# Kernel optimization log

Hardware: AMD Instinct MI355X
Metric: run time of the kernel (lower is better)

The kernel has to match this reference:

```python
import jax, jax.numpy as jnp
import numpy as np

ORDER = 2
BN_EPS = 1e-5

def setup_inputs() -> dict:
    key = jax.random.key(0)
    ks = jax.random.split(key, 8)
    B, N, L, H = 32, 512, 12, 64
    S = 2                      # support_len
    OUT = 64                   # out_dim
    M = ORDER * S * H          # einsum middle dim = 256
    x = jax.random.normal(ks[0], (B, N, L, H), dtype=jnp.float32)
    # row-scaled random diffusion matrices to keep multi-hop propagation stable
    support = jax.random.uniform(ks[1], (S, N, N), dtype=jnp.float32) / N
    scale = 1.0 / M
    weight = scale * jax.random.normal(ks[2], (L, M, OUT), dtype=jnp.float32)
    eps = jnp.zeros((1,), dtype=jnp.float32)
    gamma = jnp.ones((OUT,), dtype=jnp.float32)
    beta = jnp.zeros((OUT,), dtype=jnp.float32)
    w2 = jax.random.normal(ks[3], (OUT, OUT), dtype=jnp.float32) / np.sqrt(OUT)
    b2 = jnp.zeros((OUT,), dtype=jnp.float32)
    return {"x": x, "support": support, "weight": weight, "eps": eps,
            "gamma": gamma, "beta": beta, "w2": w2, "b2": b2}

def reference(x, support, weight, eps, gamma, beta, w2, b2):
    B, N, L, H = x.shape
    xv = x.reshape(B, N, L * H)            # [B,N,LH]
    res = []
    for i in range(support.shape[0]):      # small fixed loop over supports
        A = support[i]                     # [N,N]
        out = xv
        for _ in range(ORDER):
            out = (1.0 + eps) * out + jnp.einsum('nm,bmd->bnd', A, out)
            res.append(out)
    out = jnp.stack(res, axis=-1)          # [B,N,LH,K], K = order*support_len
    K = out.shape[-1]
    out = out.reshape(B, N, L, H * K)      # [B,N,L,M]
    out = jnp.einsum('bnlm,lmo->bno', out, weight)   # [B,N,OUT]
    # dropout is identity in eval mode
    C = out.shape[-1]
    flat = out.reshape(B * N, C)
    mean = flat.mean(axis=0)
    var = flat.var(axis=0)                 # biased, matching torch BN training
    normed = (flat - mean) * jax.lax.rsqrt(var + BN_EPS) * gamma + beta
    y = jax.nn.relu(normed.reshape(B, N, C))
    return jnp.einsum('bnc,oc->bno', y, w2) + b2
```

## Files before the change

kernel.cpp:

```cpp
#include <hip/hip_runtime.h>
#include <hip/hip_bf16.h>
#include <cstddef>
#include <cstdint>

#define B_   32
#define N_   512
#define D_   768
#define OUT_ 64
#define R_   (B_ * N_)

typedef unsigned short u16;
typedef __bf16 bf16x8 __attribute__((ext_vector_type(8)));
typedef float  f32x4  __attribute__((ext_vector_type(4)));
typedef unsigned short u16x8 __attribute__((ext_vector_type(8)));

__device__ __forceinline__ u16 f2bf(float f) {
    __hip_bfloat16 h = __float2bfloat16(f);
    return __builtin_bit_cast(u16, h);
}

__device__ __forceinline__ f32x4 mfma16(u16x8 a, u16x8 b, f32x4 c) {
    return __builtin_amdgcn_mfma_f32_16x16x32_bf16(
        __builtin_bit_cast(bf16x8, a), __builtin_bit_cast(bf16x8, b), c, 0, 0, 0);
}

__device__ __forceinline__ void gl2lds16(const void* g, void* l) {
    __builtin_amdgcn_global_load_lds(
        (const __attribute__((address_space(1))) unsigned int*)g,
        (__attribute__((address_space(3))) unsigned int*)l, 16, 0, 0);
}

__global__ __launch_bounds__(256) void prep2(
    const float* __restrict__ support, const float* __restrict__ weight,
    const float* __restrict__ epsp,
    u16* __restrict__ MallC, u16* __restrict__ MT, u16* __restrict__ Wt)
{
    const int blk = blockIdx.x, tid = threadIdx.x;
    __shared__ float t[32][33];
    if (blk < 512) {
        int s = blk >> 8, rem = blk & 255;
        int n0 = (rem >> 4) * 32, m0 = (rem & 15) * 32;
        const float f = 1.0f + epsp[0];
        const float* S = support + (size_t)s * 262144;
#pragma unroll
        for (int p = 0; p < 4; ++p) {
            int nl = p * 8 + (tid >> 5), ml = tid & 31;
            float v = S[(size_t)(n0 + nl) * 512 + m0 + ml];
            if (n0 + nl == m0 + ml) v += f;
            MallC[(size_t)(n0 + nl) * 2048 + s * 1024 + m0 + ml] = f2bf(v);
            t[nl][ml] = v;
        }
        __syncthreads();
#pragma unroll
        for (int p = 0; p < 4; ++p) {
            int ml = p * 8 + (tid >> 5), nl = tid & 31;
            MT[(size_t)s * 262144 + (size_t)(m0 + ml) * 512 + n0 + nl] = f2bf(t[nl][ml]);
        }
    } else {
        int idx = (blk - 512) * 256 + tid;
        int k = idx / 49152, rem = idx % 49152;
        int o = rem / 768, d = rem % 768;
        int l = d >> 6, hh = d & 63;
        Wt[idx] = f2bf(weight[((size_t)l * 256 + hh * 4 + k) * 64 + o]);
    }
}

__global__ __launch_bounds__(256) void zgemm_fused(
    const u16* __restrict__ Wt, const float* __restrict__ x,
    const u16* __restrict__ MallC_in, const u16* __restrict__ MT,
    u16* __restrict__ Z, u16* __restrict__ MallC_out)
{
    __shared__ __align__(16) char smem[32768];
    const int tid = threadIdx.x, lane = tid & 63, wid = tid >> 6;
    const int wr = wid >> 1, wc = wid & 1;
    const int lrow = lane & 15, lk = (lane >> 4) * 8;
    const int q = lane >> 4;
    const int bid = blockIdx.x;

    if (bid < 512) {
        u16* As = (u16*)smem;
        u16* Bs = (u16*)(smem + 16384);
        const int rt = bid >> 1, y = bid & 1;
        const int j0 = rt * 64;

        const u16* gsrcA[4]; u16* ldstA[4];
#pragma unroll
        for (int t = 0; t < 4; ++t) {
            int idx = wid * 4 + t;
            int pan = idx >> 3, sub = idx & 7;
            gsrcA[t] = Wt + (size_t)(y * 128 + sub * 16 + lrow) * 768 + pan * 32 + lk;
            ldstA[t] = As + pan * 4096 + sub * 512;
        }
        const int brow = tid & 63, kp = tid >> 6;
        const f32x4* gx = (const f32x4*)(x + (size_t)(j0 + brow) * 768 + kp * 16);
        u16* bdst = Bs + (kp >> 1) * 2048 + (brow >> 4) * 512 + (brow & 15) * 8;
        const int bo0 = (kp & 1) * 2 * 128, bo1 = bo0 + 128;

        f32x4 acc[4][2] = {};
        for (int kk = 0; kk < 12; ++kk) {
#pragma unroll
            for (int t = 0; t < 4; ++t) gl2lds16(gsrcA[t], ldstA[t]);
#pragma unroll
            for (int t = 0; t < 4; ++t) gsrcA[t] += 64;
            f32x4 a0 = gx[0], a1 = gx[1], a2 = gx[2], a3 = gx[3];
            gx += 16;
            u16x8 w0, w1;
#pragma unroll
            for (int j = 0; j < 4; ++j) {
                w0[j] = f2bf(a0[j]); w0[4 + j] = f2bf(a1[j]);
                w1[j] = f2bf(a2[j]); w1[4 + j] = f2bf(a3[j]);
            }
            *(u16x8*)(bdst + bo0) = w0;
            *(u16x8*)(bdst + bo1) = w1;
            __syncthreads();
#pragma unroll
            for (int pan = 0; pan < 2; ++pan) {
                u16x8 af[4], bq[2];
#pragma unroll
                for (int f = 0; f < 4; ++f)
                    af[f] = *(const u16x8*)(As + pan * 4096 + (wr * 4 + f) * 512 + lane * 8);
#pragma unroll
                for (int f = 0; f < 2; ++f)
                    bq[f] = *(const u16x8*)(Bs + pan * 2048 + (wc * 2 + f) * 512 + lane * 8);
#pragma unroll
                for (int fi = 0; fi < 4; ++fi)
#pragma unroll
                    for (int fj = 0; fj < 2; ++fj)
                        acc[fi][fj] = mfma16(af[fi], bq[fj], acc[fi][fj]);
            }
            __syncthreads();
        }
        u16* Rw = (u16*)smem + wid * 2560;
#pragma unroll
        for (int fi = 0; fi < 4; ++fi)
#pragma unroll
            for (int fj = 0; fj < 2; ++fj)
#pragma unroll
                for (int r = 0; r < 4; ++r)
                    Rw[(fi * 16 + q * 4 + r) * 40 + fj * 16 + lrow] = f2bf(acc[fi][fj][r]);
        __syncthreads();
        const int k = y * 2 + wr;
        const int b = rt >> 3;
        const int m0 = (j0 & 511) + wc * 32;
#pragma unroll
        for (int p = 0; p < 4; ++p) {
            int row = p * 16 + (lane >> 2);
            int cc = (lane & 3) * 8;
            u16x8 v = *(const u16x8*)(Rw + row * 40 + cc);
            *(u16x8*)(Z + (size_t)(b * 64 + row) * 2048 + k * 512 + m0 + cc) = v;
        }
    } else {
        u16* St = (u16*)smem;
        int lb = bid - 512;
        int s = lb >> 4, rem = lb & 15;
        int i0 = (rem >> 2) * 128, j0 = (rem & 3) * 128;
        const u16* Ab = MallC_in + s * 1024;
        const u16* Bb = MT + (size_t)s * 262144;

        const u16* gsrc[8]; u16* ldst[8];
#pragma unroll
        for (int t = 0; t < 8; ++t) {
            int idx = wid * 8 + t;
            int pan = idx >> 4, q2 = idx & 15;
            if (q2 < 8) {
                gsrc[t] = Ab + (size_t)(i0 + q2 * 16 + lrow) * 2048 + pan * 32 + lk;
                ldst[t] = St + pan * 8192 + q2 * 512;
            } else {
                gsrc[t] = Bb + (size_t)(j0 + (q2 - 8) * 16 + lrow) * 512 + pan * 32 + lk;
                ldst[t] = St + pan * 8192 + 4096 + (q2 - 8) * 512;
            }
        }
        f32x4 acc[4][4] = {};
        for (int kk = 0; kk < 8; ++kk) {
#pragma unroll
            for (int t = 0; t < 8; ++t) gl2lds16(gsrc[t], ldst[t]);
#pragma unroll
            for (int t = 0; t < 8; ++t) gsrc[t] += 64;
            __syncthreads();
#pragma unroll
            for (int pan = 0; pan < 2; ++pan) {
                u16x8 af[4], bq[4];
#pragma unroll
                for (int f = 0; f < 4; ++f)
                    af[f] = *(const u16x8*)(St + pan * 8192 + (wr * 4 + f) * 512 + lane * 8);
#pragma unroll
                for (int f = 0; f < 4; ++f)
                    bq[f] = *(const u16x8*)(St + pan * 8192 + 4096 + (wc * 4 + f) * 512 + lane * 8);
#pragma unroll
                for (int fi = 0; fi < 4; ++fi)
#pragma unroll
                    for (int fj = 0; fj < 4; ++fj)
                        acc[fi][fj] = mfma16(af[fi], bq[fj], acc[fi][fj]);
            }
            __syncthreads();
        }
#pragma unroll
        for (int fi = 0; fi < 4; ++fi)
#pragma unroll
            for (int fj = 0; fj < 4; ++fj)
#pragma unroll
                for (int r = 0; r < 4; ++r) {
                    int n = i0 + wr * 64 + fi * 16 + q * 4 + r;
                    int c = j0 + wc * 64 + fj * 16 + lrow;
                    MallC_out[(size_t)n * 2048 + (2 * s + 1) * 512 + c] = f2bf(acc[fi][fj][r]);
                }
    }
}

__global__ __launch_bounds__(256) void ysum(
    const u16* __restrict__ MallC, const u16* __restrict__ Z,
    float* __restrict__ Yh)
{
    __shared__ __align__(16) u16 St[8192];
    u16* As = St; u16* Bs = St + 4096;
    const int tid = threadIdx.x, lane = tid & 63, wid = tid >> 6;
    const int wr = wid >> 1, wc = wid & 1;
    const int lrow = lane & 15, lk = (lane >> 4) * 8;
    const int bid = blockIdx.x;
    const int rt = bid & 255, ks = bid >> 8;
    const int r0 = rt * 64, b = rt >> 3, n0 = r0 & 511;
    const size_t km0 = (size_t)ks * 1024;

    const u16* gsrc[4]; u16* ldst[4];
#pragma unroll
    for (int t = 0; t < 4; ++t) {
        int idx = wid * 4 + t;
        int pan = idx >> 3, q2 = idx & 7;
        if (q2 < 4) {
            gsrc[t] = MallC + (size_t)(n0 + q2 * 16 + lrow) * 2048 + km0 + pan * 32 + lk;
            ldst[t] = As + pan * 2048 + q2 * 512;
        } else {
            int s2 = q2 - 4;
            gsrc[t] = Z + (size_t)(b * 64 + s2 * 16 + lrow) * 2048 + km0 + pan * 32 + lk;
            ldst[t] = Bs + pan * 2048 + s2 * 512;
        }
    }
    f32x4 acc[2][2] = {};
    for (int kk = 0; kk < 16; ++kk) {
#pragma unroll
        for (int t = 0; t < 4; ++t) gl2lds16(gsrc[t], ldst[t]);
#pragma unroll
        for (int t = 0; t < 4; ++t) gsrc[t] += 64;
        __syncthreads();
#pragma unroll
        for (int pan = 0; pan < 2; ++pan) {
            u16x8 af[2], bq[2];
#pragma unroll
            for (int f = 0; f < 2; ++f)
                af[f] = *(const u16x8*)(As + pan * 2048 + (wr * 2 + f) * 512 + lane * 8);
#pragma unroll
            for (int f = 0; f < 2; ++f)
                bq[f] = *(const u16x8*)(Bs + pan * 2048 + (wc * 2 + f) * 512 + lane * 8);
#pragma unroll
            for (int fi = 0; fi < 2; ++fi)
#pragma unroll
                for (int fj = 0; fj < 2; ++fj)
                    acc[fi][fj] = mfma16(af[fi], bq[fj], acc[fi][fj]);
        }
        __syncthreads();
    }
    const int q = lane >> 4;
    float* Yk = Yh + (size_t)ks * R_ * 64;
#pragma unroll
    for (int fi = 0; fi < 2; ++fi)
#pragma unroll
        for (int fj = 0; fj < 2; ++fj)
#pragma unroll
            for (int r = 0; r < 4; ++r) {
                int rr = r0 + wr * 32 + fi * 16 + q * 4 + r;
                int o  = wc * 32 + fj * 16 + lrow;
                Yk[(size_t)rr * 64 + o] = acc[fi][fj][r];
            }
}

__global__ __launch_bounds__(256) void bn_part(
    const float* __restrict__ Yh, float* __restrict__ part)
{
    const int blk = blockIdx.x, tid = threadIdx.x;
    const int o = tid & 63, g = tid >> 6;
    float s = 0.f, s2 = 0.f;
#pragma unroll
    for (int p = 0; p < 16; ++p) {
        int r = blk * 64 + p * 4 + g;
        size_t off = (size_t)r * 64 + o;
        float v = Yh[off] + Yh[(size_t)R_ * 64 + off];
        s += v; s2 += v * v;
    }
    __shared__ float ls[4][64], ls2[4][64];
    ls[g][o] = s; ls2[g][o] = s2;
    __syncthreads();
    if (tid < 64) {
        float t = 0.f, t2 = 0.f;
#pragma unroll
        for (int g2 = 0; g2 < 4; ++g2) { t += ls[g2][tid]; t2 += ls2[g2][tid]; }
        part[blk * 128 + tid]      = t;
        part[blk * 128 + 64 + tid] = t2;
    }
}

__global__ __launch_bounds__(256) void bn_final(
    const float* __restrict__ part, const float* __restrict__ gamma,
    const float* __restrict__ beta, float* __restrict__ stats)
{
    const int tid = threadIdx.x;
    const int c = tid & 63, g = tid >> 6;
    float s = 0.f, s2 = 0.f;
    for (int b = g; b < 256; b += 4) {
        s  += part[b * 128 + c];
        s2 += part[b * 128 + 64 + c];
    }
    __shared__ float ls[4][64], ls2[4][64];
    ls[g][c] = s; ls2[g][c] = s2;
    __syncthreads();
    if (tid < 64) {
        float t = 0.f, t2 = 0.f;
#pragma unroll
        for (int g2 = 0; g2 < 4; ++g2) { t += ls[g2][tid]; t2 += ls2[g2][tid]; }
        float mean = t * (1.0f / R_);
        float var  = t2 * (1.0f / R_) - mean * mean;
        float a = rsqrtf(var + 1e-5f) * gamma[tid];
        stats[tid]      = a;
        stats[64 + tid] = beta[tid] - mean * a;
    }
}

__global__ __launch_bounds__(256) void bn_out(
    const float* __restrict__ Yh, const float* __restrict__ stats,
    const float* __restrict__ w2, const float* __restrict__ b2,
    float* __restrict__ out)
{
    __shared__ float ys[64 * 68];
    __shared__ float w2s[64 * 65];
    __shared__ float sa[64], sh[64];
    const int tid = threadIdx.x;
    const int r0 = blockIdx.x * 64;
#pragma unroll
    for (int i = 0; i < 16; ++i) {
        int idx = tid + i * 256;
        w2s[(idx >> 6) * 65 + (idx & 63)] = w2[idx];
    }
    if (tid < 64) { sa[tid] = stats[tid]; sh[tid] = stats[64 + tid]; }
    __syncthreads();
    const int o = tid & 63, g = tid >> 6;
    {
        float a = sa[o], b = sh[o];
#pragma unroll
        for (int p = 0; p < 16; ++p) {
            int rl = p * 4 + g;
            size_t off = (size_t)(r0 + rl) * 64 + o;
            float v = Yh[off] + Yh[(size_t)R_ * 64 + off];
            ys[o * 68 + rl] = fmaxf(fmaf(v, a, b), 0.f);
        }
    }
    __syncthreads();
    float acc[16];
    float bb = b2[o];
#pragma unroll
    for (int j = 0; j < 16; ++j) acc[j] = bb;
    for (int c = 0; c < 64; ++c) {
        float wv = w2s[o * 65 + c];
        const float* yr = ys + c * 68 + g * 16;
        f32x4 y0 = *(const f32x4*)(yr);
        f32x4 y1 = *(const f32x4*)(yr + 4);
        f32x4 y2 = *(const f32x4*)(yr + 8);
        f32x4 y3 = *(const f32x4*)(yr + 12);
#pragma unroll
        for (int j = 0; j < 4; ++j) {
            acc[j]      = fmaf(wv, y0[j], acc[j]);
            acc[4 + j]  = fmaf(wv, y1[j], acc[4 + j]);
            acc[8 + j]  = fmaf(wv, y2[j], acc[8 + j]);
            acc[12 + j] = fmaf(wv, y3[j], acc[12 + j]);
        }
    }
#pragma unroll
    for (int j = 0; j < 16; ++j)
        out[(size_t)(r0 + g * 16 + j) * OUT_ + o] = acc[j];
}

extern "C" void kernel_launch(void* const* d_in, const int* in_sizes, int n_in,
                              void* d_out, int out_size, void* d_ws, size_t ws_size,
                              hipStream_t stream)
{
    const float* x       = (const float*)d_in[0];
    const float* support = (const float*)d_in[1];
    const float* weight  = (const float*)d_in[2];
    const float* eps     = (const float*)d_in[3];
    const float* gamma   = (const float*)d_in[4];
    const float* beta    = (const float*)d_in[5];
    const float* w2      = (const float*)d_in[6];
    const float* b2      = (const float*)d_in[7];
    float* out = (float*)d_out;

    char* ws = (char*)d_ws;
    u16*   MallC = (u16*)(ws);
    u16*   MT    = (u16*)(ws + 2097152);
    u16*   Wt    = (u16*)(ws + 3145728);
    u16*   Z     = (u16*)(ws + 3538944);
    float* Yh    = (float*)(ws + 11927552);
    float* part  = (float*)(ws + 20316160);
    float* stats = (float*)(ws + 20447232);

    prep2     <<<1280, 256, 0, stream>>>(support, weight, eps, MallC, MT, Wt);
    zgemm_fused<<<544, 256, 0, stream>>>(Wt, x, MallC, MT, Z, MallC);
    ysum      <<<512,  256, 0, stream>>>(MallC, Z, Yh);
    bn_part   <<<256,  256, 0, stream>>>(Yh, part);
    bn_final  <<<1,    256, 0, stream>>>(part, gamma, beta, stats);
    bn_out    <<<256,  256, 0, stream>>>(Yh, stats, w2, b2, out);
}
```

Measured before the change: 172.7 us.

## Pre-convert x to bf16 and software-pipeline GEMM LDS loads with multi-buffering

Moves the fp32→bf16 conversion of x into the prep kernel, writing a bf16 copy to workspace so the Z GEMM can stream it with direct global-to-LDS loads. The Z GEMM gets double-buffered LDS with vmcnt waits and raw barriers. ysum gets triple-buffered prefetch two tiles ahead. Block indices are also remapped so related tiles share an XCD. This aims to hide global load latency behind MFMA work, at the cost of an extra full pass over x (read fp32, write bf16) and more shared memory per block.

```diff
diff --git a/kernel.cpp b/kernel.cpp
--- a/kernel.cpp
+++ b/kernel.cpp
@@ -14,6 +14,9 @@
 typedef float  f32x4  __attribute__((ext_vector_type(4)));
 typedef unsigned short u16x8 __attribute__((ext_vector_type(8)));
 
+#define WAITVM(n) __asm__ __volatile__("s_waitcnt vmcnt(" #n ")" ::: "memory")
+#define SBAR()    __builtin_amdgcn_s_barrier()
+
 __device__ __forceinline__ u16 f2bf(float f) {
     __hip_bfloat16 h = __float2bfloat16(f);
     return __builtin_bit_cast(u16, h);
@@ -30,15 +33,25 @@
         (__attribute__((address_space(3))) unsigned int*)l, 16, 0, 0);
 }
 
-__global__ __launch_bounds__(256) void prep2(
-    const float* __restrict__ support, const float* __restrict__ weight,
-    const float* __restrict__ epsp,
-    u16* __restrict__ MallC, u16* __restrict__ MT, u16* __restrict__ Wt)
+__global__ __launch_bounds__(256) void prep3(
+    const float* __restrict__ x, const float* __restrict__ support,
+    const float* __restrict__ weight, const float* __restrict__ epsp,
+    u16* __restrict__ xb, u16* __restrict__ MallC, u16* __restrict__ MT,
+    u16* __restrict__ Wt)
 {
     const int blk = blockIdx.x, tid = threadIdx.x;
     __shared__ float t[32][33];
-    if (blk < 512) {
-        int s = blk >> 8, rem = blk & 255;
+    if (blk < 6144) {
+        int i = (blk * 256 + tid) * 8;
+        f32x4 a = *(const f32x4*)(x + i);
+        f32x4 b = *(const f32x4*)(x + i + 4);
+        u16x8 o;
+#pragma unroll
+        for (int j = 0; j < 4; ++j) { o[j] = f2bf(a[j]); o[4 + j] = f2bf(b[j]); }
+        *(u16x8*)(xb + i) = o;
+    } else if (blk < 6656) {
+        int local = blk - 6144;
+        int s = local >> 8, rem = local & 255;
         int n0 = (rem >> 4) * 32, m0 = (rem & 15) * 32;
         const float f = 1.0f + epsp[0];
         const float* S = support + (size_t)s * 262144;
@@ -57,7 +70,7 @@
             MT[(size_t)s * 262144 + (size_t)(m0 + ml) * 512 + n0 + nl] = f2bf(t[nl][ml]);
         }
     } else {
-        int idx = (blk - 512) * 256 + tid;
+        int idx = (blk - 6656) * 256 + tid;
         int k = idx / 49152, rem = idx % 49152;
         int o = rem / 768, d = rem % 768;
         int l = d >> 6, hh = d & 63;
@@ -65,12 +78,13 @@
     }
 }
 
-__global__ __launch_bounds__(256) void zgemm_fused(
-    const u16* __restrict__ Wt, const float* __restrict__ x,
+__global__ __launch_bounds__(256) void zmsq(
+    const u16* __restrict__ Wt, const u16* __restrict__ xb,
     const u16* __restrict__ MallC_in, const u16* __restrict__ MT,
     u16* __restrict__ Z, u16* __restrict__ MallC_out)
 {
-    __shared__ __align__(16) char smem[32768];
+    __shared__ __align__(16) char smem[49152];
+    u16* SM = (u16*)smem;
     const int tid = threadIdx.x, lane = tid & 63, wid = tid >> 6;
     const int wr = wid >> 1, wc = wid & 1;
     const int lrow = lane & 15, lk = (lane >> 4) * 8;
@@ -78,57 +92,57 @@
     const int bid = blockIdx.x;
 
     if (bid < 512) {
-        u16* As = (u16*)smem;
-        u16* Bs = (u16*)(smem + 16384);
-        const int rt = bid >> 1, y = bid & 1;
-        const int j0 = rt * 64;
-
-        const u16* gsrcA[4]; u16* ldstA[4];
-#pragma unroll
-        for (int t = 0; t < 4; ++t) {
-            int idx = wid * 4 + t;
-            int pan = idx >> 3, sub = idx & 7;
-            gsrcA[t] = Wt + (size_t)(y * 128 + sub * 16 + lrow) * 768 + pan * 32 + lk;
-            ldstA[t] = As + pan * 4096 + sub * 512;
-        }
-        const int brow = tid & 63, kp = tid >> 6;
-        const f32x4* gx = (const f32x4*)(x + (size_t)(j0 + brow) * 768 + kp * 16);
-        u16* bdst = Bs + (kp >> 1) * 2048 + (brow >> 4) * 512 + (brow & 15) * 8;
-        const int bo0 = (kp & 1) * 2 * 128, bo1 = bo0 + 128;
+        const int j = bid & 7, y = (bid >> 3) & 1, g = bid >> 4;
+        const int rt = g * 8 + j;
+        const int b = rt >> 3;
+
+        const u16* gsrc[6]; int loff[6];
+#pragma unroll
+        for (int t = 0; t < 6; ++t) {
+            int idx = wid * 6 + t;
+            if (idx < 16) {
+                int pan = idx >> 3, sub = idx & 7;
+                gsrc[t] = Wt + (size_t)(y * 128 + sub * 16 + lrow) * 768 + pan * 32 + lk;
+                loff[t] = pan * 4096 + sub * 512;
+            } else {
+                int i2 = idx - 16;
+                int pan = i2 >> 2, sub = i2 & 3;
+                gsrc[t] = xb + (size_t)(rt * 64 + sub * 16 + lrow) * 768 + pan * 32 + lk;
+                loff[t] = 8192 + pan * 2048 + sub * 512;
+            }
+        }
+#pragma unroll
+        for (int t = 0; t < 6; ++t) { gl2lds16(gsrc[t], SM + loff[t]); gsrc[t] += 64; }
 
         f32x4 acc[4][2] = {};
+#pragma unroll
         for (int kk = 0; kk < 12; ++kk) {
-#pragma unroll
-            for (int t = 0; t < 4; ++t) gl2lds16(gsrcA[t], ldstA[t]);
-#pragma unroll
-            for (int t = 0; t < 4; ++t) gsrcA[t] += 64;
-            f32x4 a0 = gx[0], a1 = gx[1], a2 = gx[2], a3 = gx[3];
-            gx += 16;
-            u16x8 w0, w1;
-#pragma unroll
-            for (int j = 0; j < 4; ++j) {
-                w0[j] = f2bf(a0[j]); w0[4 + j] = f2bf(a1[j]);
-                w1[j] = f2bf(a2[j]); w1[4 + j] = f2bf(a3[j]);
-            }
-            *(u16x8*)(bdst + bo0) = w0;
-            *(u16x8*)(bdst + bo1) = w1;
-            __syncthreads();
+            if (kk < 11) {
+                u16* base = SM + ((kk + 1) & 1) * 12288;
+#pragma unroll
+                for (int t = 0; t < 6; ++t) { gl2lds16(gsrc[t], base + loff[t]); gsrc[t] += 64; }
+                WAITVM(6);
+            } else {
+                WAITVM(0);
+            }
+            SBAR();
+            const u16* base = SM + (kk & 1) * 12288;
 #pragma unroll
             for (int pan = 0; pan < 2; ++pan) {
                 u16x8 af[4], bq[2];
 #pragma unroll
                 for (int f = 0; f < 4; ++f)
-                    af[f] = *(const u16x8*)(As + pan * 4096 + (wr * 4 + f) * 512 + lane * 8);
+                    af[f] = *(const u16x8*)(base + pan * 4096 + (wr * 4 + f) * 512 + lane * 8);
 #pragma unroll
                 for (int f = 0; f < 2; ++f)
-                    bq[f] = *(const u16x8*)(Bs + pan * 2048 + (wc * 2 + f) * 512 + lane * 8);
+                    bq[f] = *(const u16x8*)(base + 8192 + pan * 2048 + (wc * 2 + f) * 512 + lane * 8);
 #pragma unroll
                 for (int fi = 0; fi < 4; ++fi)
 #pragma unroll
                     for (int fj = 0; fj < 2; ++fj)
                         acc[fi][fj] = mfma16(af[fi], bq[fj], acc[fi][fj]);
             }
-            __syncthreads();
+            SBAR();
         }
         u16* Rw = (u16*)smem + wid * 2560;
 #pragma unroll
@@ -140,8 +154,7 @@
                     Rw[(fi * 16 + q * 4 + r) * 40 + fj * 16 + lrow] = f2bf(acc[fi][fj][r]);
         __syncthreads();
         const int k = y * 2 + wr;
-        const int b = rt >> 3;
-        const int m0 = (j0 & 511) + wc * 32;
+        const int m0 = (rt & 7) * 64 + wc * 32;
 #pragma unroll
         for (int p = 0; p < 4; ++p) {
             int row = p * 16 + (lane >> 2);
@@ -150,7 +163,7 @@
             *(u16x8*)(Z + (size_t)(b * 64 + row) * 2048 + k * 512 + m0 + cc) = v;
         }
     } else {
-        u16* St = (u16*)smem;
+        u16* St = SM;
         int lb = bid - 512;
         int s = lb >> 4, rem = lb & 15;
         int i0 = (rem >> 2) * 128, j0 = (rem & 3) * 128;
@@ -211,53 +224,68 @@
     const u16* __restrict__ MallC, const u16* __restrict__ Z,
     float* __restrict__ Yh)
 {
-    __shared__ __align__(16) u16 St[8192];
-    u16* As = St; u16* Bs = St + 4096;
+    __shared__ __align__(16) u16 SM[24576];
     const int tid = threadIdx.x, lane = tid & 63, wid = tid >> 6;
     const int wr = wid >> 1, wc = wid & 1;
     const int lrow = lane & 15, lk = (lane >> 4) * 8;
     const int bid = blockIdx.x;
-    const int rt = bid & 255, ks = bid >> 8;
-    const int r0 = rt * 64, b = rt >> 3, n0 = r0 & 511;
+    const int xcd = bid & 7, tt = bid >> 3;
+    const int b = (tt >> 4) * 8 + xcd;
+    const int nt = (tt >> 1) & 7, ks = tt & 1;
+    const int n0 = nt * 64;
+    const int r0 = b * 512 + n0;
     const size_t km0 = (size_t)ks * 1024;
 
-    const u16* gsrc[4]; u16* ldst[4];
+    const u16* gsrc[4]; int loff[4];
 #pragma unroll
     for (int t = 0; t < 4; ++t) {
         int idx = wid * 4 + t;
-        int pan = idx >> 3, q2 = idx & 7;
-        if (q2 < 4) {
-            gsrc[t] = MallC + (size_t)(n0 + q2 * 16 + lrow) * 2048 + km0 + pan * 32 + lk;
-            ldst[t] = As + pan * 2048 + q2 * 512;
+        if (idx < 8) {
+            int pan = idx >> 2, sub = idx & 3;
+            gsrc[t] = MallC + (size_t)(n0 + sub * 16 + lrow) * 2048 + km0 + pan * 32 + lk;
+            loff[t] = pan * 2048 + sub * 512;
         } else {
-            int s2 = q2 - 4;
-            gsrc[t] = Z + (size_t)(b * 64 + s2 * 16 + lrow) * 2048 + km0 + pan * 32 + lk;
-            ldst[t] = Bs + pan * 2048 + s2 * 512;
-        }
+            int i2 = idx - 8;
+            int pan = i2 >> 2, sub = i2 & 3;
+            gsrc[t] = Z + (size_t)(b * 64 + sub * 16 + lrow) * 2048 + km0 + pan * 32 + lk;
+            loff[t] = 4096 + pan * 2048 + sub * 512;
+        }
+    }
+#pragma unroll
+    for (int st = 0; st < 2; ++st) {
+#pragma unroll
+        for (int t = 0; t < 4; ++t) { gl2lds16(gsrc[t], SM + st * 8192 + loff[t]); gsrc[t] += 64; }
     }
     f32x4 acc[2][2] = {};
+#pragma unroll
     for (int kk = 0; kk < 16; ++kk) {
-#pragma unroll
-        for (int t = 0; t < 4; ++t) gl2lds16(gsrc[t], ldst[t]);
-#pragma unroll
-        for (int t = 0; t < 4; ++t) gsrc[t] += 64;
-        __syncthreads();
+        int nxt = kk + 2;
+        if (nxt < 16) {
+            u16* base = SM + (nxt % 3) * 8192;
+#pragma unroll
+            for (int t = 0; t < 4; ++t) { gl2lds16(gsrc[t], base + loff[t]); gsrc[t] += 64; }
+        }
+        if (kk < 14) WAITVM(8);
+        else if (kk == 14) WAITVM(4);
+        else WAITVM(0);
+        SBAR();
+        const u16* base = SM + (kk % 3) * 8192;
 #pragma unroll
         for (int pan = 0; pan < 2; ++pan) {
             u16x8 af[2], bq[2];
 #pragma unroll
             for (int f = 0; f < 2; ++f)
-                af[f] = *(const u16x8*)(As + pan * 2048 + (wr * 2 + f) * 512 + lane * 8);
+                af[f] = *(const u16x8*)(base + pan * 2048 + (wr * 2 + f) * 512 + lane * 8);
 #pragma unroll
             for (int f = 0; f < 2; ++f)
-                bq[f] = *(const u16x8*)(Bs + pan * 2048 + (wc * 2 + f) * 512 + lane * 8);
+                bq[f] = *(const u16x8*)(base + 4096 + pan * 2048 + (wc * 2 + f) * 512 + lane * 8);
 #pragma unroll
             for (int fi = 0; fi < 2; ++fi)
 #pragma unroll
                 for (int fj = 0; fj < 2; ++fj)
                     acc[fi][fj] = mfma16(af[fi], bq[fj], acc[fi][fj]);
         }
-        __syncthreads();
+        SBAR();
     }
     const int q = lane >> 4;
     float* Yk = Yh + (size_t)ks * R_ * 64;
@@ -392,18 +420,19 @@
     float* out = (float*)d_out;
 
     char* ws = (char*)d_ws;
-    u16*   MallC = (u16*)(ws);
-    u16*   MT    = (u16*)(ws + 2097152);
-    u16*   Wt    = (u16*)(ws + 3145728);
-    u16*   Z     = (u16*)(ws + 3538944);
-    float* Yh    = (float*)(ws + 11927552);
-    float* part  = (float*)(ws + 20316160);
-    float* stats = (float*)(ws + 20447232);
-
-    prep2     <<<1280, 256, 0, stream>>>(support, weight, eps, MallC, MT, Wt);
-    zgemm_fused<<<544, 256, 0, stream>>>(Wt, x, MallC, MT, Z, MallC);
-    ysum      <<<512,  256, 0, stream>>>(MallC, Z, Yh);
-    bn_part   <<<256,  256, 0, stream>>>(Yh, part);
-    bn_final  <<<1,    256, 0, stream>>>(part, gamma, beta, stats);
-    bn_out    <<<256,  256, 0, stream>>>(Yh, stats, w2, b2, out);
-}
+    u16*   xb    = (u16*)(ws);
+    u16*   MallC = (u16*)(ws + 25165824);
+    u16*   MT    = (u16*)(ws + 27262976);
+    u16*   Wt    = (u16*)(ws + 28311552);
+    u16*   Z     = (u16*)(ws + 28704768);
+    float* Yh    = (float*)(ws + 37093376);
+    float* part  = (float*)(ws + 45481984);
+    float* stats = (float*)(ws + 45613056);
+
+    prep3   <<<7424, 256, 0, stream>>>(x, support, weight, eps, xb, MallC, MT, Wt);
+    zmsq    <<<544,  256, 0, stream>>>(Wt, xb, MallC, MT, Z, MallC);
+    ysum    <<<512,  256, 0, stream>>>(MallC, Z, Yh);
+    bn_part <<<256,  256, 0, stream>>>(Yh, part);
+    bn_final<<<1,    256, 0, stream>>>(part, gamma, beta, stats);
+    bn_out  <<<256,  256, 0, stream>>>(Yh, stats, w2, b2, out);
+}
```

Result: no change. 175.8 us (+1.8%).

## Load GEMM operands directly to registers with prefetch and 4-way split-K ysum

Applied to the files above, without the earlier changes.

The Z GEMM and the ysum GEMM no longer stage operands through LDS with block barriers. Each wave now loads its MFMA fragments straight from global memory into registers and prefetches the next k-step while the current one computes. ysum's tiling changes to 128-row by 64-column tiles with a 4-way K split instead of 2-way, so the BN kernels now sum four partial Yh buffers. This removes LDS traffic and syncs, but gives up cross-wave reuse of loaded tiles and writes and reads extra partial-sum memory.

```diff
diff --git a/kernel.cpp b/kernel.cpp
--- a/kernel.cpp
+++ b/kernel.cpp
@@ -65,70 +65,69 @@
     }
 }
 
-__global__ __launch_bounds__(256) void zgemm_fused(
+__global__ __launch_bounds__(256) void zmsq(
     const u16* __restrict__ Wt, const float* __restrict__ x,
     const u16* __restrict__ MallC_in, const u16* __restrict__ MT,
     u16* __restrict__ Z, u16* __restrict__ MallC_out)
 {
     __shared__ __align__(16) char smem[32768];
     const int tid = threadIdx.x, lane = tid & 63, wid = tid >> 6;
-    const int wr = wid >> 1, wc = wid & 1;
-    const int lrow = lane & 15, lk = (lane >> 4) * 8;
+    const int lrow = lane & 15, lk8 = (lane >> 4) * 8;
     const int q = lane >> 4;
     const int bid = blockIdx.x;
 
     if (bid < 512) {
-        u16* As = (u16*)smem;
-        u16* Bs = (u16*)(smem + 16384);
-        const int rt = bid >> 1, y = bid & 1;
-        const int j0 = rt * 64;
-
-        const u16* gsrcA[4]; u16* ldstA[4];
-#pragma unroll
-        for (int t = 0; t < 4; ++t) {
-            int idx = wid * 4 + t;
-            int pan = idx >> 3, sub = idx & 7;
-            gsrcA[t] = Wt + (size_t)(y * 128 + sub * 16 + lrow) * 768 + pan * 32 + lk;
-            ldstA[t] = As + pan * 4096 + sub * 512;
-        }
-        const int brow = tid & 63, kp = tid >> 6;
-        const f32x4* gx = (const f32x4*)(x + (size_t)(j0 + brow) * 768 + kp * 16);
-        u16* bdst = Bs + (kp >> 1) * 2048 + (brow >> 4) * 512 + (brow & 15) * 8;
-        const int bo0 = (kp & 1) * 2 * 128, bo1 = bo0 + 128;
+        const int y = bid & 1, mt = bid >> 1;
+        const int b = mt >> 3, m0 = (mt & 7) * 64;
+        const int wr = wid >> 1, wc = wid & 1;
+
+        const u16* ap[4];
+#pragma unroll
+        for (int fi = 0; fi < 4; ++fi)
+            ap[fi] = Wt + (size_t)(y * 128 + wr * 64 + fi * 16 + lrow) * 768 + lk8;
+        const float* bp[2];
+#pragma unroll
+        for (int fj = 0; fj < 2; ++fj)
+            bp[fj] = x + (size_t)(b * 512 + m0 + wc * 32 + fj * 16 + lrow) * 768 + lk8;
+
+        u16x8 Ar[4]; f32x4 Br0[2], Br1[2];
+#pragma unroll
+        for (int fi = 0; fi < 4; ++fi) Ar[fi] = *(const u16x8*)(ap[fi]);
+#pragma unroll
+        for (int fj = 0; fj < 2; ++fj) {
+            Br0[fj] = *(const f32x4*)(bp[fj]);
+            Br1[fj] = *(const f32x4*)(bp[fj] + 4);
+        }
 
         f32x4 acc[4][2] = {};
-        for (int kk = 0; kk < 12; ++kk) {
-#pragma unroll
-            for (int t = 0; t < 4; ++t) gl2lds16(gsrcA[t], ldstA[t]);
-#pragma unroll
-            for (int t = 0; t < 4; ++t) gsrcA[t] += 64;
-            f32x4 a0 = gx[0], a1 = gx[1], a2 = gx[2], a3 = gx[3];
-            gx += 16;
-            u16x8 w0, w1;
-#pragma unroll
-            for (int j = 0; j < 4; ++j) {
-                w0[j] = f2bf(a0[j]); w0[4 + j] = f2bf(a1[j]);
-                w1[j] = f2bf(a2[j]); w1[4 + j] = f2bf(a3[j]);
+#pragma unroll
+        for (int kk = 0; kk < 24; ++kk) {
+            u16x8 Bc[2];
+#pragma unroll
+            for (int fj = 0; fj < 2; ++fj) {
+                u16x8 w;
+#pragma unroll
+                for (int j = 0; j < 4; ++j) { w[j] = f2bf(Br0[fj][j]); w[4 + j] = f2bf(Br1[fj][j]); }
+                Bc[fj] = w;
             }
-            *(u16x8*)(bdst + bo0) = w0;
-            *(u16x8*)(bdst + bo1) = w1;
-            __syncthreads();
-#pragma unroll
-            for (int pan = 0; pan < 2; ++pan) {
-                u16x8 af[4], bq[2];
-#pragma unroll
-                for (int f = 0; f < 4; ++f)
-                    af[f] = *(const u16x8*)(As + pan * 4096 + (wr * 4 + f) * 512 + lane * 8);
-#pragma unroll
-                for (int f = 0; f < 2; ++f)
-                    bq[f] = *(const u16x8*)(Bs + pan * 2048 + (wc * 2 + f) * 512 + lane * 8);
-#pragma unroll
-                for (int fi = 0; fi < 4; ++fi)
-#pragma unroll
-                    for (int fj = 0; fj < 2; ++fj)
-                        acc[fi][fj] = mfma16(af[fi], bq[fj], acc[fi][fj]);
+            u16x8 Ac[4];
+#pragma unroll
+            for (int fi = 0; fi < 4; ++fi) Ac[fi] = Ar[fi];
+            if (kk < 23) {
+                const int d = (kk + 1) * 32;
+#pragma unroll
+                for (int fi = 0; fi < 4; ++fi) Ar[fi] = *(const u16x8*)(ap[fi] + d);
+#pragma unroll
+                for (int fj = 0; fj < 2; ++fj) {
+                    Br0[fj] = *(const f32x4*)(bp[fj] + d);
+                    Br1[fj] = *(const f32x4*)(bp[fj] + d + 4);
+                }
             }
-            __syncthreads();
+#pragma unroll
+            for (int fi = 0; fi < 4; ++fi)
+#pragma unroll
+                for (int fj = 0; fj < 2; ++fj)
+                    acc[fi][fj] = mfma16(Ac[fi], Bc[fj], acc[fi][fj]);
         }
         u16* Rw = (u16*)smem + wid * 2560;
 #pragma unroll
@@ -140,17 +139,16 @@
                     Rw[(fi * 16 + q * 4 + r) * 40 + fj * 16 + lrow] = f2bf(acc[fi][fj][r]);
         __syncthreads();
         const int k = y * 2 + wr;
-        const int b = rt >> 3;
-        const int m0 = (j0 & 511) + wc * 32;
 #pragma unroll
         for (int p = 0; p < 4; ++p) {
             int row = p * 16 + (lane >> 2);
             int cc = (lane & 3) * 8;
             u16x8 v = *(const u16x8*)(Rw + row * 40 + cc);
-            *(u16x8*)(Z + (size_t)(b * 64 + row) * 2048 + k * 512 + m0 + cc) = v;
+            *(u16x8*)(Z + (size_t)(b * 64 + row) * 2048 + k * 512 + m0 + wc * 32 + cc) = v;
         }
     } else {
         u16* St = (u16*)smem;
+        const int wr = wid >> 1, wc = wid & 1;
         int lb = bid - 512;
         int s = lb >> 4, rem = lb & 15;
         int i0 = (rem >> 2) * 128, j0 = (rem & 3) * 128;
@@ -163,10 +161,10 @@
             int idx = wid * 8 + t;
             int pan = idx >> 4, q2 = idx & 15;
             if (q2 < 8) {
-                gsrc[t] = Ab + (size_t)(i0 + q2 * 16 + lrow) * 2048 + pan * 32 + lk;
+                gsrc[t] = Ab + (size_t)(i0 + q2 * 16 + lrow) * 2048 + pan * 32 + lk8;
                 ldst[t] = St + pan * 8192 + q2 * 512;
             } else {
-                gsrc[t] = Bb + (size_t)(j0 + (q2 - 8) * 16 + lrow) * 512 + pan * 32 + lk;
+                gsrc[t] = Bb + (size_t)(j0 + (q2 - 8) * 16 + lrow) * 512 + pan * 32 + lk8;
                 ldst[t] = St + pan * 8192 + 4096 + (q2 - 8) * 512;
             }
         }
@@ -208,67 +206,61 @@
 }
 
 __global__ __launch_bounds__(256) void ysum(
-    const u16* __restrict__ MallC, const u16* __restrict__ Z,
-    float* __restrict__ Yh)
-{
-    __shared__ __align__(16) u16 St[8192];
-    u16* As = St; u16* Bs = St + 4096;
+    const u16* __restrict__ G, const u16* __restrict__ Z, float* __restrict__ Yh)
+{
     const int tid = threadIdx.x, lane = tid & 63, wid = tid >> 6;
-    const int wr = wid >> 1, wc = wid & 1;
-    const int lrow = lane & 15, lk = (lane >> 4) * 8;
+    const int lrow = lane & 15, lk8 = (lane >> 4) * 8;
+    const int q = lane >> 4;
     const int bid = blockIdx.x;
-    const int rt = bid & 255, ks = bid >> 8;
-    const int r0 = rt * 64, b = rt >> 3, n0 = r0 & 511;
-    const size_t km0 = (size_t)ks * 1024;
-
-    const u16* gsrc[4]; u16* ldst[4];
-#pragma unroll
-    for (int t = 0; t < 4; ++t) {
-        int idx = wid * 4 + t;
-        int pan = idx >> 3, q2 = idx & 7;
-        if (q2 < 4) {
-            gsrc[t] = MallC + (size_t)(n0 + q2 * 16 + lrow) * 2048 + km0 + pan * 32 + lk;
-            ldst[t] = As + pan * 2048 + q2 * 512;
-        } else {
-            int s2 = q2 - 4;
-            gsrc[t] = Z + (size_t)(b * 64 + s2 * 16 + lrow) * 2048 + km0 + pan * 32 + lk;
-            ldst[t] = Bs + pan * 2048 + s2 * 512;
-        }
-    }
-    f32x4 acc[2][2] = {};
+    const int kq = bid & 3, rt = bid >> 2;
+    const int b = rt >> 2, n0 = (rt & 3) * 128;
+    const int r0 = b * 512 + n0;
+
+    const u16* ap[2];
+#pragma unroll
+    for (int fi = 0; fi < 2; ++fi)
+        ap[fi] = G + (size_t)(n0 + wid * 32 + fi * 16 + lrow) * 2048 + kq * 512 + lk8;
+    const u16* bp[4];
+#pragma unroll
+    for (int fj = 0; fj < 4; ++fj)
+        bp[fj] = Z + (size_t)(b * 64 + fj * 16 + lrow) * 2048 + kq * 512 + lk8;
+
+    u16x8 Ar[2], Br[4];
+#pragma unroll
+    for (int fi = 0; fi < 2; ++fi) Ar[fi] = *(const u16x8*)(ap[fi]);
+#pragma unroll
+    for (int fj = 0; fj < 4; ++fj) Br[fj] = *(const u16x8*)(bp[fj]);
+
+    f32x4 acc[2][4] = {};
+#pragma unroll
     for (int kk = 0; kk < 16; ++kk) {
-#pragma unroll
-        for (int t = 0; t < 4; ++t) gl2lds16(gsrc[t], ldst[t]);
-#pragma unroll
-        for (int t = 0; t < 4; ++t) gsrc[t] += 64;
-        __syncthreads();
-#pragma unroll
-        for (int pan = 0; pan < 2; ++pan) {
-            u16x8 af[2], bq[2];
-#pragma unroll
-            for (int f = 0; f < 2; ++f)
-                af[f] = *(const u16x8*)(As + pan * 2048 + (wr * 2 + f) * 512 + lane * 8);
-#pragma unroll
-            for (int f = 0; f < 2; ++f)
-                bq[f] = *(const u16x8*)(Bs + pan * 2048 + (wc * 2 + f) * 512 + lane * 8);
-#pragma unroll
-            for (int fi = 0; fi < 2; ++fi)
-#pragma unroll
-                for (int fj = 0; fj < 2; ++fj)
-                    acc[fi][fj] = mfma16(af[fi], bq[fj], acc[fi][fj]);
-        }
-        __syncthreads();
-    }
-    const int q = lane >> 4;
-    float* Yk = Yh + (size_t)ks * R_ * 64;
+        u16x8 Ac[2], Bc[4];
+#pragma unroll
+        for (int fi = 0; fi < 2; ++fi) Ac[fi] = Ar[fi];
+#pragma unroll
+        for (int fj = 0; fj < 4; ++fj) Bc[fj] = Br[fj];
+        if (kk < 15) {
+            const int d = (kk + 1) * 32;
+#pragma unroll
+            for (int fi = 0; fi < 2; ++fi) Ar[fi] = *(const u16x8*)(ap[fi] + d);
+#pragma unroll
+            for (int fj = 0; fj < 4; ++fj) Br[fj] = *(const u16x8*)(bp[fj] + d);
+        }
+#pragma unroll
+        for (int fi = 0; fi < 2; ++fi)
+#pragma unroll
+            for (int fj = 0; fj < 4; ++fj)
+                acc[fi][fj] = mfma16(Ac[fi], Bc[fj], acc[fi][fj]);
+    }
+    float* Yk = Yh + (size_t)kq * R_ * 64;
 #pragma unroll
     for (int fi = 0; fi < 2; ++fi)
 #pragma unroll
-        for (int fj = 0; fj < 2; ++fj)
+        for (int fj = 0; fj < 4; ++fj)
 #pragma unroll
             for (int r = 0; r < 4; ++r) {
-                int rr = r0 + wr * 32 + fi * 16 + q * 4 + r;
-                int o  = wc * 32 + fj * 16 + lrow;
+                int rr = r0 + wid * 32 + fi * 16 + q * 4 + r;
+                int o  = fj * 16 + lrow;
                 Yk[(size_t)rr * 64 + o] = acc[fi][fj][r];
             }
 }
@@ -283,7 +275,8 @@
     for (int p = 0; p < 16; ++p) {
         int r = blk * 64 + p * 4 + g;
         size_t off = (size_t)r * 64 + o;
-        float v = Yh[off] + Yh[(size_t)R_ * 64 + off];
+        float v = Yh[off] + Yh[(size_t)R_ * 64 + off]
+                + Yh[(size_t)2 * R_ * 64 + off] + Yh[(size_t)3 * R_ * 64 + off];
         s += v; s2 += v * v;
     }
     __shared__ float ls[4][64], ls2[4][64];
@@ -343,13 +336,14 @@
     __syncthreads();
     const int o = tid & 63, g = tid >> 6;
     {
-        float a = sa[o], b = sh[o];
+        float a = sa[o], bsh = sh[o];
 #pragma unroll
         for (int p = 0; p < 16; ++p) {
             int rl = p * 4 + g;
             size_t off = (size_t)(r0 + rl) * 64 + o;
-            float v = Yh[off] + Yh[(size_t)R_ * 64 + off];
-            ys[o * 68 + rl] = fmaxf(fmaf(v, a, b), 0.f);
+            float v = Yh[off] + Yh[(size_t)R_ * 64 + off]
+                    + Yh[(size_t)2 * R_ * 64 + off] + Yh[(size_t)3 * R_ * 64 + off];
+            ys[o * 68 + rl] = fmaxf(fmaf(v, a, bsh), 0.f);
         }
     }
     __syncthreads();
@@ -397,13 +391,13 @@
     u16*   Wt    = (u16*)(ws + 3145728);
     u16*   Z     = (u16*)(ws + 3538944);
     float* Yh    = (float*)(ws + 11927552);
-    float* part  = (float*)(ws + 20316160);
-    float* stats = (float*)(ws + 20447232);
-
-    prep2     <<<1280, 256, 0, stream>>>(support, weight, eps, MallC, MT, Wt);
-    zgemm_fused<<<544, 256, 0, stream>>>(Wt, x, MallC, MT, Z, MallC);
-    ysum      <<<512,  256, 0, stream>>>(MallC, Z, Yh);
-    bn_part   <<<256,  256, 0, stream>>>(Yh, part);
-    bn_final  <<<1,    256, 0, stream>>>(part, gamma, beta, stats);
-    bn_out    <<<256,  256, 0, stream>>>(Yh, stats, w2, b2, out);
-}
+    float* part  = (float*)(ws + 28704768);
+    float* stats = (float*)(ws + 28835840);
+
+    prep2   <<<1280, 256, 0, stream>>>(support, weight, eps, MallC, MT, Wt);
+    zmsq    <<<544,  256, 0, stream>>>(Wt, x, MallC, MT, Z, MallC);
+    ysum    <<<512,  256, 0, stream>>>(MallC, Z, Yh);
+    bn_part <<<256,  256, 0, stream>>>(Yh, part);
+    bn_final<<<1,    256, 0, stream>>>(part, gamma, beta, stats);
+    bn_out  <<<256,  256, 0, stream>>>(Yh, stats, w2, b2, out);
+}
```

Result: slower. 203.5 us (+17.8%).
